# Optimization experiments

Hardware: AMD Instinct MI355X
Metric: run time of the kernel (lower is better)

The kernel has to match this reference:

```python
import jax, jax.numpy as jnp
import numpy as np

N, E, D, H, G, OUT = 50000, 800000, 128, 128, 64, 10


def setup_inputs() -> dict:
    key = jax.random.key(0)
    ks = jax.random.split(key, 10)
    x = jax.random.normal(ks[0], (N, D), dtype=jnp.float32)
    edge_index = jax.random.randint(ks[1], (2, E), 0, N, dtype=jnp.int64)
    batch = jnp.sort(jax.random.randint(ks[2], (N,), 0, G, dtype=jnp.int64))
    s = 1.0 / np.sqrt(D)
    W0 = jax.random.normal(ks[3], (D, H), dtype=jnp.float32) * s
    W1 = jax.random.normal(ks[4], (H, H), dtype=jnp.float32) * s
    W2 = jax.random.normal(ks[5], (H, H), dtype=jnp.float32) * s
    M0w = jax.random.normal(ks[6], (H, H), dtype=jnp.float32) * s
    M0b = jnp.zeros((H,), dtype=jnp.float32)
    M1w = jax.random.normal(ks[7], (H, OUT), dtype=jnp.float32) * s
    M1b = jnp.zeros((OUT,), dtype=jnp.float32)
    return dict(x=x, W0=W0, W1=W1, W2=W2, M0w=M0w, M0b=M0b, M1w=M1w, M1b=M1b,
                edge_index=edge_index, batch=batch)


def gcn_conv(x, W, src, dst):
    # PyG GCNConv (bias=False): h = x @ W; out = D^-1/2 (A + I) D^-1/2 h
    h = x @ W
    deg = jnp.zeros((N,), h.dtype).at[dst].add(1.0) + 1.0  # +1 for self-loop
    dinv = deg ** -0.5
    w = dinv[src] * dinv[dst]  # [E]
    agg = jax.ops.segment_sum(h[src] * w[:, None], dst, num_segments=N)
    return agg + h * (dinv * dinv)[:, None]  # self-loop term


def reference(x, W0, W1, W2, M0w, M0b, M1w, M1b, edge_index, batch):
    src, dst = edge_index[0], edge_index[1]
    h = gcn_conv(x, W0, src, dst)
    h = gcn_conv(jax.nn.relu(h), W1, src, dst)
    h = gcn_conv(jax.nn.relu(h), W2, src, dst)
    # global mean pool over graphs
    sums = jax.ops.segment_sum(h, batch, num_segments=G)
    cnts = jax.ops.segment_sum(jnp.ones((N,), h.dtype), batch, num_segments=G)
    pooled = sums / jnp.maximum(cnts, 1.0)[:, None]
    out = pooled @ M0w + M0b
    out = jax.nn.relu(out) @ M1w + M1b
    return out
```

## Files before the change

kernel.cpp:

```cpp
#include <hip/hip_runtime.h>
#include <hip/hip_fp16.h>

#define NN 50000
#define NE 800000
#define DIM 128
#define NG 64
#define NOUT 10

#define NBKT 391
#define HBLK 256
#define CHUNK ((NE + HBLK - 1) / HBLK)

#define NPB 16
#define AGB (NN / NPB)

#define WPAD 136
#define PSTR (DIM * WPAD)

typedef __attribute__((ext_vector_type(8))) short short8;
typedef __attribute__((ext_vector_type(8))) _Float16 half8;
typedef __attribute__((ext_vector_type(4))) float float4v;

union S8H8 { short8 s; half8 h; };
union SH { short s; _Float16 h; };

#define PREP_WB 48
#define PREP_HB (PREP_WB + HBLK)
#define PREP_NB (PREP_HB + 1)
__global__ __launch_bounds__(256) void prep_kernel(const float* __restrict__ W0,
                                                   const float* __restrict__ W1,
                                                   const float* __restrict__ W2,
                                                   short* __restrict__ wsp,
                                                   const int* __restrict__ ei,
                                                   int* __restrict__ blkhist,
                                                   const int* __restrict__ batch,
                                                   int* __restrict__ first,
                                                   float* __restrict__ pools) {
    __shared__ int h[NBKT];
    int bx = blockIdx.x;
    if (bx < PREP_WB) {
        int w = bx >> 4;
        int sub = bx & 15;
        const float* W = (w == 0) ? W0 : (w == 1) ? W1 : W2;
        short* Wp = wsp + w * PSTR;
        #pragma unroll
        for (int t = 0; t < 4; ++t) {
            int idx = sub * 1024 + t * 256 + threadIdx.x;
            int k = idx >> 7, n = idx & 127;
            int phys = n * WPAD + k;
            SH c;
            c.h = (_Float16)W[idx];
            Wp[phys] = c.s;
        }
    } else if (bx < PREP_HB) {
        int b = bx - PREP_WB;
        for (int i = threadIdx.x; i < NBKT; i += 256) h[i] = 0;
        __syncthreads();
        int lo = b * CHUNK, hi = min(lo + CHUNK, NE);
        for (int e = lo + threadIdx.x; e < hi; e += 256)
            atomicAdd(&h[ei[NE + e] >> 7], 1);
        __syncthreads();
        for (int i = threadIdx.x; i < NBKT; i += 256)
            blkhist[b * NBKT + i] = h[i];
    } else {
        int g = threadIdx.x;
        if (g <= NG) {
            int lo = 0, hi = NN;
            while (lo < hi) {
                int mid = (lo + hi) >> 1;
                if (batch[mid] < g) lo = mid + 1; else hi = mid;
            }
            first[g] = lo;
        }
        for (int i = threadIdx.x; i < NG * DIM; i += 256) pools[i] = 0.0f;
    }
}

__global__ __launch_bounds__(256) void scan_all(int* __restrict__ blkhist,
                                                int* __restrict__ bintot) {
    __shared__ int s[256];
    int bin = blockIdx.x;
    int t = threadIdx.x;
    int v = blkhist[t * NBKT + bin];
    s[t] = v;
    __syncthreads();
    #pragma unroll
    for (int off = 1; off < 256; off <<= 1) {
        int tv = (t >= off) ? s[t - off] : 0;
        __syncthreads();
        s[t] += tv;
        __syncthreads();
    }
    blkhist[t * NBKT + bin] = s[t] - v;
    if (t == 255) bintot[bin] = s[255];
}

__device__ __forceinline__ void local_base_scan(const int* __restrict__ bintot,
                                                int* a , int* ps ,
                                                int* base ) {
    int t = threadIdx.x & 255;
    a[2 * t]     = (2 * t < NBKT)     ? bintot[2 * t]     : 0;
    a[2 * t + 1] = (2 * t + 1 < NBKT) ? bintot[2 * t + 1] : 0;
    __syncthreads();
    int loc = a[2 * t] + a[2 * t + 1];
    ps[t] = loc;
    __syncthreads();
    #pragma unroll
    for (int off = 1; off < 256; off <<= 1) {
        int tv = (t >= off) ? ps[t - off] : 0;
        __syncthreads();
        ps[t] += tv;
        __syncthreads();
    }
    int excl = ps[t] - loc;
    base[2 * t] = excl;
    base[2 * t + 1] = excl + a[2 * t];
    __syncthreads();
}

__global__ __launch_bounds__(256) void scatter_gemm(const int* __restrict__ ei,
                                                    const int* __restrict__ blkhist,
                                                    const int* __restrict__ bintot,
                                                    unsigned* __restrict__ ebuf,
                                                    const float* __restrict__ X,
                                                    const short* __restrict__ Wsp,
                                                    __half* __restrict__ Y) {
    __shared__ int a[512];
    __shared__ int ps[256];
    __shared__ int base[512];
    __shared__ int cur[NBKT];
    int bx = blockIdx.x;
    if (bx < HBLK) {
        local_base_scan(bintot, a, ps, base);
        for (int i = threadIdx.x; i < NBKT; i += 256)
            cur[i] = blkhist[bx * NBKT + i] + base[i];
        __syncthreads();
        int lo = bx * CHUNK, hi = min(lo + CHUNK, NE);
        for (int e = lo + threadIdx.x; e < hi; e += 256) {
            int s = ei[e];
            int d = ei[NE + e];
            int pos = atomicAdd(&cur[d >> 7], 1);
            ebuf[pos] = ((unsigned)(d & 127) << 16) | (unsigned)s;
        }
    } else {
        int tid = threadIdx.x;
        int wave = tid >> 6;
        int lane = tid & 63;
        int lm = lane & 15;
        int lq = lane >> 4;
        int row0 = (bx - HBLK) * 64 + wave * 16;
        float4v acc[8];
        #pragma unroll
        for (int i = 0; i < 8; ++i) acc[i] = (float4v){0.f, 0.f, 0.f, 0.f};
        #pragma unroll
        for (int kk = 0; kk < 4; ++kk) {
            int r = min(row0 + lm, NN - 1);
            const float* ap = X + (size_t)r * DIM + kk * 32 + lq * 8;
            float4 xa = *(const float4*)ap;
            float4 xb = *(const float4*)(ap + 4);
            half8 av;
            av[0] = (_Float16)xa.x; av[1] = (_Float16)xa.y;
            av[2] = (_Float16)xa.z; av[3] = (_Float16)xa.w;
            av[4] = (_Float16)xb.x; av[5] = (_Float16)xb.y;
            av[6] = (_Float16)xb.z; av[7] = (_Float16)xb.w;
            const short* bp = Wsp + kk * 32 + lq * 8;
            #pragma unroll
            for (int n0 = 0; n0 < 8; ++n0) {
                S8H8 b;
                b.s = *(const short8*)(bp + (lm * 8 + n0) * WPAD);
                acc[n0] = __builtin_amdgcn_mfma_f32_16x16x32_f16(av, b.h, acc[n0], 0, 0, 0);
            }
        }
        #pragma unroll
        for (int rg = 0; rg < 4; ++rg) {
            int row = row0 + lq * 4 + rg;
            if (row < NN) {
                short8 o;
                #pragma unroll
                for (int j = 0; j < 8; ++j) {
                    SH c;
                    c.h = (_Float16)acc[j][rg];
                    o[j] = c.s;
                }
                *(short8*)((short*)Y + (size_t)row * DIM + lm * 8) = o;
            }
        }
    }
}

__global__ __launch_bounds__(256) void build_csr(const unsigned* __restrict__ ebuf,
                                                 const int* __restrict__ bintot,
                                                 int* __restrict__ rowoff,
                                                 int* __restrict__ csr_src,
                                                 float* __restrict__ dinv) {
    __shared__ int a[512];
    __shared__ int ps[256];
    __shared__ int base[512];
    __shared__ int deg[128];
    __shared__ int loff[128];
    int g = blockIdx.x;
    int t = threadIdx.x;
    local_base_scan(bintot, a, ps, base);
    int lo = base[g];
    int hi = (g + 1 < NBKT) ? base[g + 1] : NE;
    if (t < 128) deg[t] = 0;
    __syncthreads();
    for (int p = lo + t; p < hi; p += 256)
        atomicAdd(&deg[ebuf[p] >> 16], 1);
    __syncthreads();
    int v = (t < 128) ? deg[t] : 0;
    if (t < 128) loff[t] = v;
    __syncthreads();
    #pragma unroll
    for (int off = 1; off < 128; off <<= 1) {
        int tv = (t < 128 && t >= off) ? loff[t - off] : 0;
        __syncthreads();
        if (t < 128) loff[t] += tv;
        __syncthreads();
    }
    if (t < 128) {
        int excl = loff[t] - v;
        int node = g * 128 + t;
        if (node < NN) {
            rowoff[node] = lo + excl;
            dinv[node] = 1.0f / sqrtf((float)v + 1.0f);
        }
        if (node == 0) rowoff[NN] = NE;
        deg[t] = lo + excl;
    }
    __syncthreads();
    for (int p = lo + t; p < hi; p += 256) {
        unsigned pk = ebuf[p];
        int pos = atomicAdd(&deg[pk >> 16], 1);
        csr_src[pos] = (int)(pk & 0xFFFFu);
    }
}

template <bool RELU>
__device__ __forceinline__ void gather_node(const __half* __restrict__ Hc,
                                            const int* __restrict__ rowoff,
                                            const int* __restrict__ csr_src,
                                            const float* __restrict__ dinv,
                                            int i, short8* o) {
    int s = rowoff[i], e = rowoff[i + 1];
    float di = dinv[i];
    short8 qs = *(const short8*)(Hc + (size_t)i * DIM);
    float acc1[8] = {0.f, 0.f, 0.f, 0.f, 0.f, 0.f, 0.f, 0.f};
    int p = s;
    for (; p + 3 < e; p += 4) {
        int u0 = csr_src[p];
        int u1 = csr_src[p + 1];
        int u2 = csr_src[p + 2];
        int u3 = csr_src[p + 3];
        float d0 = dinv[u0], d1 = dinv[u1], d2 = dinv[u2], d3 = dinv[u3];
        short8 q0 = *(const short8*)(Hc + (size_t)u0 * DIM);
        short8 q1 = *(const short8*)(Hc + (size_t)u1 * DIM);
        short8 q2 = *(const short8*)(Hc + (size_t)u2 * DIM);
        short8 q3 = *(const short8*)(Hc + (size_t)u3 * DIM);
        #pragma unroll
        for (int k = 0; k < 8; ++k) {
            acc1[k] = fmaf(d0, __half2float(((const __half*)&q0)[k]), acc1[k]);
            acc1[k] = fmaf(d1, __half2float(((const __half*)&q1)[k]), acc1[k]);
            acc1[k] = fmaf(d2, __half2float(((const __half*)&q2)[k]), acc1[k]);
            acc1[k] = fmaf(d3, __half2float(((const __half*)&q3)[k]), acc1[k]);
        }
    }
    for (; p < e; ++p) {
        int u = csr_src[p];
        float d = dinv[u];
        short8 q = *(const short8*)(Hc + (size_t)u * DIM);
        #pragma unroll
        for (int k = 0; k < 8; ++k)
            acc1[k] = fmaf(d, __half2float(((const __half*)&q)[k]), acc1[k]);
    }
    #pragma unroll
    for (int k = 0; k < 8; ++k) {
        float v = di * fmaf(di, __half2float(((const __half*)&qs)[k]), acc1[k]);
        if (RELU) v = fmaxf(v, 0.0f);
        SH c; c.h = (_Float16)v;
        (*o)[k] = c.s;
    }
}

__global__ __launch_bounds__(256) void agg_gemm(const __half* __restrict__ H,
                                                const short* __restrict__ Wsp,
                                                __half* __restrict__ Y,
                                                const int* __restrict__ rowoff,
                                                const int* __restrict__ csr_src,
                                                const float* __restrict__ dinv) {
    __shared__ short A_s[NPB][WPAD];
    int tid = threadIdx.x;
    int nb = blockIdx.x * NPB;
    {
        int g = tid >> 4;
        int ln = tid & 15;
        short8 o;
        gather_node<true>(H + ln * 8, rowoff, csr_src, dinv, nb + g, &o);
        *(short8*)&A_s[g][ln * 8] = o;
    }
    __syncthreads();
    if (tid >= 64) return;
    int lm = tid & 15;
    int lq = tid >> 4;
    float4v acc[8];
    #pragma unroll
    for (int i = 0; i < 8; ++i) acc[i] = (float4v){0.f, 0.f, 0.f, 0.f};
    #pragma unroll
    for (int kk = 0; kk < 4; ++kk) {
        S8H8 av;
        av.s = *(const short8*)&A_s[lm][kk * 32 + lq * 8];
        const short* bp = Wsp + kk * 32 + lq * 8;
        #pragma unroll
        for (int n0 = 0; n0 < 8; ++n0) {
            S8H8 b;
            b.s = *(const short8*)(bp + (lm * 8 + n0) * WPAD);
            acc[n0] = __builtin_amdgcn_mfma_f32_16x16x32_f16(av.h, b.h, acc[n0], 0, 0, 0);
        }
    }
    #pragma unroll
    for (int rg = 0; rg < 4; ++rg) {
        int row = nb + lq * 4 + rg;
        short8 o;
        #pragma unroll
        for (int j = 0; j < 8; ++j) {
            SH c;
            c.h = (_Float16)acc[j][rg];
            o[j] = c.s;
        }
        *(short8*)((short*)Y + (size_t)row * DIM + lm * 8) = o;
    }
}

__global__ __launch_bounds__(256) void agg_pool(const __half* __restrict__ H,
                                                const int* __restrict__ rowoff,
                                                const int* __restrict__ csr_src,
                                                const float* __restrict__ dinv,
                                                const int* __restrict__ batch,
                                                float* __restrict__ pools) {
    __shared__ short A_s[NPB][WPAD];
    __shared__ int gb[NPB];
    int tid = threadIdx.x;
    int nb = blockIdx.x * NPB;
    if (tid < NPB) gb[tid] = batch[nb + tid];
    {
        int g = tid >> 4;
        int ln = tid & 15;
        short8 o;
        gather_node<false>(H + ln * 8, rowoff, csr_src, dinv, nb + g, &o);
        *(short8*)&A_s[g][ln * 8] = o;
    }
    __syncthreads();
    int c = tid & 127;
    int hf = tid >> 7;
    int r0 = hf * 8;
    float acc = 0.f;
    int cg = gb[r0];
    for (int r = r0; r < r0 + 8; ++r) {
        int g2 = gb[r];
        if (g2 != cg) {
            atomicAdd(&pools[cg * DIM + c], acc);
            acc = 0.f;
            cg = g2;
        }
        SH u;
        u.s = A_s[r][c];
        acc += (float)u.h;
    }
    atomicAdd(&pools[cg * DIM + c], acc);
}

__global__ __launch_bounds__(128) void mlp_kernel(const float* __restrict__ pools,
                                                  const int* __restrict__ first,
                                                  const float* __restrict__ M0w,
                                                  const float* __restrict__ M0b,
                                                  const float* __restrict__ M1w,
                                                  const float* __restrict__ M1b,
                                                  float* __restrict__ out) {
    __shared__ float p[DIM];
    __shared__ float t[DIM];
    int g = blockIdx.x;
    int j = threadIdx.x;
    float cnt = (float)max(first[g + 1] - first[g], 1);
    p[j] = pools[g * DIM + j] / cnt;
    __syncthreads();
    float acc = M0b[j];
    #pragma unroll 8
    for (int k = 0; k < DIM; ++k) acc = fmaf(p[k], M0w[k * DIM + j], acc);
    t[j] = fmaxf(acc, 0.0f);
    __syncthreads();
    if (j < NOUT) {
        float o = M1b[j];
        #pragma unroll 8
        for (int k = 0; k < DIM; ++k) o = fmaf(t[k], M1w[k * NOUT + j], o);
        out[g * NOUT + j] = o;
    }
}

extern "C" void kernel_launch(void* const* d_in, const int* in_sizes, int n_in,
                              void* d_out, int out_size, void* d_ws, size_t ws_size,
                              hipStream_t stream) {
    const float* x   = (const float*)d_in[0];
    const float* W0  = (const float*)d_in[1];
    const float* W1  = (const float*)d_in[2];
    const float* W2  = (const float*)d_in[3];
    const float* M0w = (const float*)d_in[4];
    const float* M0b = (const float*)d_in[5];
    const float* M1w = (const float*)d_in[6];
    const float* M1b = (const float*)d_in[7];
    const int* ei    = (const int*)d_in[8];
    const int* batch = (const int*)d_in[9];
    float* out = (float*)d_out;

    char* ws = (char*)d_ws;
    size_t off = 0;
    auto take = [&](size_t bytes) -> void* {
        void* p = ws + off;
        off = (off + bytes + 255) & ~(size_t)255;
        return p;
    };
    __half* hA   = (__half*)take((size_t)NN * DIM * 2);
    __half* hB   = (__half*)take((size_t)NN * DIM * 2);
    unsigned* ebuf = (unsigned*)take((size_t)NE * 4);
    int* csr_src = (int*)take((size_t)NE * 4);
    int* blkhist = (int*)take((size_t)HBLK * NBKT * 4);
    int* bintot  = (int*)take((size_t)NBKT * 4);
    int* rowoff  = (int*)take((size_t)(NN + 1) * 4);
    float* dinv  = (float*)take((size_t)NN * 4);
    int* first   = (int*)take((size_t)(NG + 1) * 4);
    float* pools = (float*)take((size_t)NG * DIM * 4);
    short* wsp   = (short*)take((size_t)3 * PSTR * 2);
    (void)ws_size; (void)in_sizes; (void)n_in; (void)out_size;

    const int GB = (NN + 63) / 64;

    prep_kernel<<<PREP_NB, 256, 0, stream>>>(W0, W1, W2, wsp, ei, blkhist, batch, first, pools);
    scan_all<<<NBKT, 256, 0, stream>>>(blkhist, bintot);
    scatter_gemm<<<HBLK + GB, 256, 0, stream>>>(ei, blkhist, bintot, ebuf, x, wsp, hA);
    build_csr<<<NBKT, 256, 0, stream>>>(ebuf, bintot, rowoff, csr_src, dinv);

    agg_gemm<<<AGB, 256, 0, stream>>>(hA, wsp + PSTR, hB, rowoff, csr_src, dinv);
    agg_gemm<<<AGB, 256, 0, stream>>>(hB, wsp + 2 * PSTR, hA, rowoff, csr_src, dinv);
    agg_pool<<<AGB, 256, 0, stream>>>(hA, rowoff, csr_src, dinv, batch, pools);

    mlp_kernel<<<NG, 128, 0, stream>>>(pools, first, M0w, M0b, M1w, M1b, out);
}
```

Baseline: 246.6 us.

## Replace two-pass edge bucketing with fixed-capacity buckets and global atomic offsets

Drops the separate histogram pass in prep_kernel and the scan_all kernel. Each scatter block now builds its own local histogram, reserves space per bucket with a global atomicAdd into fixed-capacity slots (BCAP per bucket), then scatters its edges. build_csr scans the per-bucket counts to get compacted CSR offsets. This removes one kernel launch and the blkhist traffic. In exchange it assumes no bucket of 128 destination nodes ever holds more than 2560 edges. That holds for uniformly random graphs, but a skewed graph would overflow silently.

```diff
diff --git a/kernel.cpp b/kernel.cpp
--- a/kernel.cpp
+++ b/kernel.cpp
@@ -10,6 +10,7 @@
 #define NBKT 391
 #define HBLK 256
 #define CHUNK ((NE + HBLK - 1) / HBLK)
+#define BCAP 2560
 
 #define NPB 16
 #define AGB (NN / NPB)
@@ -25,18 +26,15 @@
 union SH { short s; _Float16 h; };
 
 #define PREP_WB 48
-#define PREP_HB (PREP_WB + HBLK)
-#define PREP_NB (PREP_HB + 1)
+#define PREP_NB (PREP_WB + 1)
 __global__ __launch_bounds__(256) void prep_kernel(const float* __restrict__ W0,
                                                    const float* __restrict__ W1,
                                                    const float* __restrict__ W2,
                                                    short* __restrict__ wsp,
-                                                   const int* __restrict__ ei,
-                                                   int* __restrict__ blkhist,
                                                    const int* __restrict__ batch,
                                                    int* __restrict__ first,
-                                                   float* __restrict__ pools) {
-    __shared__ int h[NBKT];
+                                                   float* __restrict__ pools,
+                                                   int* __restrict__ cnt) {
     int bx = blockIdx.x;
     if (bx < PREP_WB) {
         int w = bx >> 4;
@@ -52,16 +50,6 @@
             c.h = (_Float16)W[idx];
             Wp[phys] = c.s;
         }
-    } else if (bx < PREP_HB) {
-        int b = bx - PREP_WB;
-        for (int i = threadIdx.x; i < NBKT; i += 256) h[i] = 0;
-        __syncthreads();
-        int lo = b * CHUNK, hi = min(lo + CHUNK, NE);
-        for (int e = lo + threadIdx.x; e < hi; e += 256)
-            atomicAdd(&h[ei[NE + e] >> 7], 1);
-        __syncthreads();
-        for (int i = threadIdx.x; i < NBKT; i += 256)
-            blkhist[b * NBKT + i] = h[i];
     } else {
         int g = threadIdx.x;
         if (g <= NG) {
@@ -73,73 +61,35 @@
             first[g] = lo;
         }
         for (int i = threadIdx.x; i < NG * DIM; i += 256) pools[i] = 0.0f;
-    }
-}
-
-__global__ __launch_bounds__(256) void scan_all(int* __restrict__ blkhist,
-                                                int* __restrict__ bintot) {
-    __shared__ int s[256];
-    int bin = blockIdx.x;
-    int t = threadIdx.x;
-    int v = blkhist[t * NBKT + bin];
-    s[t] = v;
-    __syncthreads();
-    #pragma unroll
-    for (int off = 1; off < 256; off <<= 1) {
-        int tv = (t >= off) ? s[t - off] : 0;
-        __syncthreads();
-        s[t] += tv;
-        __syncthreads();
-    }
-    blkhist[t * NBKT + bin] = s[t] - v;
-    if (t == 255) bintot[bin] = s[255];
-}
-
-__device__ __forceinline__ void local_base_scan(const int* __restrict__ bintot,
-                                                int* a , int* ps ,
-                                                int* base ) {
-    int t = threadIdx.x & 255;
-    a[2 * t]     = (2 * t < NBKT)     ? bintot[2 * t]     : 0;
-    a[2 * t + 1] = (2 * t + 1 < NBKT) ? bintot[2 * t + 1] : 0;
-    __syncthreads();
-    int loc = a[2 * t] + a[2 * t + 1];
-    ps[t] = loc;
-    __syncthreads();
-    #pragma unroll
-    for (int off = 1; off < 256; off <<= 1) {
-        int tv = (t >= off) ? ps[t - off] : 0;
-        __syncthreads();
-        ps[t] += tv;
-        __syncthreads();
-    }
-    int excl = ps[t] - loc;
-    base[2 * t] = excl;
-    base[2 * t + 1] = excl + a[2 * t];
-    __syncthreads();
+        for (int i = threadIdx.x; i < NBKT; i += 256) cnt[i] = 0;
+    }
 }
 
 __global__ __launch_bounds__(256) void scatter_gemm(const int* __restrict__ ei,
-                                                    const int* __restrict__ blkhist,
-                                                    const int* __restrict__ bintot,
+                                                    int* __restrict__ cnt,
                                                     unsigned* __restrict__ ebuf,
                                                     const float* __restrict__ X,
                                                     const short* __restrict__ Wsp,
                                                     __half* __restrict__ Y) {
-    __shared__ int a[512];
-    __shared__ int ps[256];
-    __shared__ int base[512];
-    __shared__ int cur[NBKT];
+    __shared__ int h[NBKT];
     int bx = blockIdx.x;
     if (bx < HBLK) {
-        local_base_scan(bintot, a, ps, base);
-        for (int i = threadIdx.x; i < NBKT; i += 256)
-            cur[i] = blkhist[bx * NBKT + i] + base[i];
+        for (int i = threadIdx.x; i < NBKT; i += 256) h[i] = 0;
         __syncthreads();
         int lo = bx * CHUNK, hi = min(lo + CHUNK, NE);
+        for (int e = lo + threadIdx.x; e < hi; e += 256)
+            atomicAdd(&h[ei[NE + e] >> 7], 1);
+        __syncthreads();
+        for (int i = threadIdx.x; i < NBKT; i += 256) {
+            int c = h[i];
+            int base = (c > 0) ? atomicAdd(&cnt[i], c) : 0;
+            h[i] = i * BCAP + base;
+        }
+        __syncthreads();
         for (int e = lo + threadIdx.x; e < hi; e += 256) {
             int s = ei[e];
             int d = ei[NE + e];
-            int pos = atomicAdd(&cur[d >> 7], 1);
+            int pos = atomicAdd(&h[d >> 7], 1);
             ebuf[pos] = ((unsigned)(d & 127) << 16) | (unsigned)s;
         }
     } else {
@@ -188,8 +138,31 @@
     }
 }
 
+__device__ __forceinline__ void local_base_scan(const int* __restrict__ cnt,
+                                                int* a , int* ps ,
+                                                int* base ) {
+    int t = threadIdx.x & 255;
+    a[2 * t]     = (2 * t < NBKT)     ? cnt[2 * t]     : 0;
+    a[2 * t + 1] = (2 * t + 1 < NBKT) ? cnt[2 * t + 1] : 0;
+    __syncthreads();
+    int loc = a[2 * t] + a[2 * t + 1];
+    ps[t] = loc;
+    __syncthreads();
+    #pragma unroll
+    for (int off = 1; off < 256; off <<= 1) {
+        int tv = (t >= off) ? ps[t - off] : 0;
+        __syncthreads();
+        ps[t] += tv;
+        __syncthreads();
+    }
+    int excl = ps[t] - loc;
+    base[2 * t] = excl;
+    base[2 * t + 1] = excl + a[2 * t];
+    __syncthreads();
+}
+
 __global__ __launch_bounds__(256) void build_csr(const unsigned* __restrict__ ebuf,
-                                                 const int* __restrict__ bintot,
+                                                 const int* __restrict__ cnt,
                                                  int* __restrict__ rowoff,
                                                  int* __restrict__ csr_src,
                                                  float* __restrict__ dinv) {
@@ -200,12 +173,13 @@
     __shared__ int loff[128];
     int g = blockIdx.x;
     int t = threadIdx.x;
-    local_base_scan(bintot, a, ps, base);
-    int lo = base[g];
-    int hi = (g + 1 < NBKT) ? base[g + 1] : NE;
+    local_base_scan(cnt, a, ps, base);
+    int gbase = base[g];
+    int rlo = g * BCAP;
+    int rhi = rlo + cnt[g];
     if (t < 128) deg[t] = 0;
     __syncthreads();
-    for (int p = lo + t; p < hi; p += 256)
+    for (int p = rlo + t; p < rhi; p += 256)
         atomicAdd(&deg[ebuf[p] >> 16], 1);
     __syncthreads();
     int v = (t < 128) ? deg[t] : 0;
@@ -222,14 +196,14 @@
         int excl = loff[t] - v;
         int node = g * 128 + t;
         if (node < NN) {
-            rowoff[node] = lo + excl;
+            rowoff[node] = gbase + excl;
             dinv[node] = 1.0f / sqrtf((float)v + 1.0f);
         }
         if (node == 0) rowoff[NN] = NE;
-        deg[t] = lo + excl;
-    }
-    __syncthreads();
-    for (int p = lo + t; p < hi; p += 256) {
+        deg[t] = gbase + excl;
+    }
+    __syncthreads();
+    for (int p = rlo + t; p < rhi; p += 256) {
         unsigned pk = ebuf[p];
         int pos = atomicAdd(&deg[pk >> 16], 1);
         csr_src[pos] = (int)(pk & 0xFFFFu);
@@ -420,10 +394,9 @@
     };
     __half* hA   = (__half*)take((size_t)NN * DIM * 2);
     __half* hB   = (__half*)take((size_t)NN * DIM * 2);
-    unsigned* ebuf = (unsigned*)take((size_t)NE * 4);
+    unsigned* ebuf = (unsigned*)take((size_t)NBKT * BCAP * 4);
     int* csr_src = (int*)take((size_t)NE * 4);
-    int* blkhist = (int*)take((size_t)HBLK * NBKT * 4);
-    int* bintot  = (int*)take((size_t)NBKT * 4);
+    int* cnt     = (int*)take((size_t)NBKT * 4);
     int* rowoff  = (int*)take((size_t)(NN + 1) * 4);
     float* dinv  = (float*)take((size_t)NN * 4);
     int* first   = (int*)take((size_t)(NG + 1) * 4);
@@ -433,10 +406,9 @@
 
     const int GB = (NN + 63) / 64;
 
-    prep_kernel<<<PREP_NB, 256, 0, stream>>>(W0, W1, W2, wsp, ei, blkhist, batch, first, pools);
-    scan_all<<<NBKT, 256, 0, stream>>>(blkhist, bintot);
-    scatter_gemm<<<HBLK + GB, 256, 0, stream>>>(ei, blkhist, bintot, ebuf, x, wsp, hA);
-    build_csr<<<NBKT, 256, 0, stream>>>(ebuf, bintot, rowoff, csr_src, dinv);
+    prep_kernel<<<PREP_NB, 256, 0, stream>>>(W0, W1, W2, wsp, batch, first, pools, cnt);
+    scatter_gemm<<<HBLK + GB, 256, 0, stream>>>(ei, cnt, ebuf, x, wsp, hA);
+    build_csr<<<NBKT, 256, 0, stream>>>(ebuf, cnt, rowoff, csr_src, dinv);
 
     agg_gemm<<<AGB, 256, 0, stream>>>(hA, wsp + PSTR, hB, rowoff, csr_src, dinv);
     agg_gemm<<<AGB, 256, 0, stream>>>(hB, wsp + 2 * PSTR, hA, rowoff, csr_src, dinv);
```

After: 247.8 us. Within noise of the previous version (+0.5%).
